# Kernel tuning notes

Hardware: AMD Instinct MI355X
Metric: run time of the kernel (lower is better)

## Reference

```python
import jax, jax.numpy as jnp
import numpy as np

B, S, T, E, D = 16, 2048, 1024, 256, 256  # batch, src_len, tgt_len, enc_size, dec_size


def setup_inputs() -> dict:
    key = jax.random.key(0)
    k1, k2, k3, k4, k5 = jax.random.split(key, 5)
    enc_states = jax.random.normal(k1, (B, S, E), dtype=jnp.float32)
    dec_states = jax.random.normal(k2, (B, T, D), dtype=jnp.float32)
    # valid-prefix mask: each row has at least one valid (True) source position
    lengths = jax.random.randint(k3, (B,), 1, S + 1)
    src_mask = jnp.arange(S)[None, :] < lengths[:, None]  # (B, S) bool
    # Dense layer weights (no bias). Glorot-ish scale.
    W_enc = jax.random.normal(k4, (E, D), dtype=jnp.float32) / np.sqrt(E)
    W_fin = jax.random.normal(k5, (E + D, D), dtype=jnp.float32) / np.sqrt(E + D)
    return {"enc_states": enc_states, "dec_states": dec_states,
            "src_mask": src_mask, "W_enc": W_enc, "W_fin": W_fin}


def reference(enc_states, dec_states, src_mask, W_enc, W_fin):
    # enc_trnsfrmr: (B,S,E) @ (E,D) -> (B,S,D)
    enc_proj = jnp.einsum('bse,ed->bsd', enc_states, W_enc)
    # attention scores: batch_dot(dec_states, enc_proj^T) -> (B,T,S)
    scores = jnp.einsum('btd,bsd->bts', dec_states, enc_proj)
    scores = jnp.where(src_mask[:, None, :], scores, -jnp.inf)
    wts = jax.nn.softmax(scores, axis=-1)  # (B,T,S)
    # broadcast-multiply + reduce_sum == weighted sum over src positions
    context = jnp.einsum('bts,bse->bte', wts, enc_states)  # (B,T,E)
    cat = jnp.concatenate([context, dec_states], axis=-1)  # (B,T,E+D)
    return jnp.tanh(jnp.einsum('btf,fd->btd', cat, W_fin))  # (B,T,D)
```

## Files before the change

kernel.cpp:

```cpp
#include <hip/hip_runtime.h>
#include <math.h>
#include <stdint.h>

#define NB 16
#define NS 2048
#define NT 1024
#define NE 256
#define ND 256
#define NM (NB * NT)
#define KF (NE + ND)

typedef short sh8 __attribute__((ext_vector_type(8)));
typedef float f4v __attribute__((ext_vector_type(4)));

static __device__ __forceinline__ float bf2f(unsigned short u) {
    union { unsigned int i; float f; } v;
    v.i = ((unsigned int)u) << 16;
    return v.f;
}
static __device__ __forceinline__ unsigned short f2bf(float f) {
    union { unsigned int i; float f; } v;
    v.f = f;
    unsigned int x = v.i;
    x += 0x7FFFu + ((x >> 16) & 1u);
    return (unsigned short)(x >> 16);
}
static __device__ __forceinline__ float4 load4(const void* p, int isbf, long idx) {
    if (isbf) {
        const unsigned short* h = (const unsigned short*)p + idx;
        ushort4 u = *(const ushort4*)h;
        return make_float4(bf2f(u.x), bf2f(u.y), bf2f(u.z), bf2f(u.w));
    }
    const float* f = (const float*)p + idx;
    return *(const float4*)f;
}
static __device__ __forceinline__ int mvalid(const void* m, int kind, int b, int s) {
    long idx = (long)b * NS + s;
    switch (kind) {
        case 0:  return ((const unsigned char*)m)[idx] != 0;
        case 1:  return ((const int*)m)[idx] != 0;
        case 2:  return ((const unsigned short*)m)[idx] != 0;
        default: return ((const unsigned int*)m)[idx] != 0;
    }
}

__global__ void k_detect(const void* __restrict__ enc_raw,
                         const void* __restrict__ mask_raw,
                         int* __restrict__ flags) {
    __shared__ int cnt;
    if (threadIdx.x == 0) cnt = 0;
    __syncthreads();
    const unsigned short* h = (const unsigned short*)enc_raw;
    int local = 0;
    for (int i = threadIdx.x; i < 4096; i += 256) {
        int ex = (h[i] >> 7) & 0xFF;
        if (ex >= 97 && ex <= 157) local++;
    }
    atomicAdd(&cnt, local);
    __syncthreads();
    if (threadIdx.x == 0) {
        int isbf = (cnt >= 3700) ? 1 : 0;
        const unsigned char* mb = (const unsigned char*)mask_raw;
        int kind;
        if (mb[1] == 0x3F)                       kind = 2;
        else if (mb[3] == 0x3F && mb[1] == 0)    kind = 3;
        else if (mb[1] == 1)                     kind = 0;
        else if (mb[4] == 1 || mb[8] == 1)       kind = 1;
        else                                     kind = (mb[NS] == 1) ? 0 : 1;
        flags[0] = isbf;
        flags[1] = kind;
    }
}

__global__ __launch_bounds__(256) void k_split(const void* __restrict__ src,
                                               const int* __restrict__ flags,
                                               unsigned short* __restrict__ hh,
                                               unsigned short* __restrict__ ll) {
    const int isbf = flags[0];
    const long i = ((long)blockIdx.x * 256 + threadIdx.x) * 8;
    if (isbf) {
        sh8 v = *(const sh8*)((const unsigned short*)src + i);
        *(sh8*)(hh + i) = v;
    } else {
        const float* f = (const float*)src + i;
        sh8 hv, lv;
#pragma unroll
        for (int j = 0; j < 8; ++j) {
            float x = f[j];
            unsigned short h = f2bf(x);
            hv[j] = (short)h;
            lv[j] = (short)f2bf(x - bf2f(h));
        }
        *(sh8*)(hh + i) = hv;
        *(sh8*)(ll + i) = lv;
    }
}

__global__ __launch_bounds__(256) void k_twf(const void* __restrict__ Wfin,
                                             const int* __restrict__ flags,
                                             unsigned short* __restrict__ wfh,
                                             unsigned short* __restrict__ wfl) {
    const int isbf = flags[0];
    __shared__ float T[64][68];
    const int f0 = blockIdx.x * 64, n0 = blockIdx.y * 64;
    const int tid = threadIdx.x;
#pragma unroll
    for (int i = 0; i < 4; ++i) {
        int idx = tid + i * 256;
        int r = idx >> 4, c4 = (idx & 15) << 2;
        float4 v = load4(Wfin, isbf, (long)(f0 + r) * ND + n0 + c4);
        T[r][c4] = v.x; T[r][c4 + 1] = v.y; T[r][c4 + 2] = v.z; T[r][c4 + 3] = v.w;
    }
    __syncthreads();
#pragma unroll
    for (int i = 0; i < 4; ++i) {
        int idx = tid + i * 256;
        int n = idx >> 4, f4 = (idx & 15) << 2;
        ushort4 hv, lv;
        float x;
        x = T[f4 + 0][n]; hv.x = f2bf(x); lv.x = f2bf(x - bf2f(hv.x));
        x = T[f4 + 1][n]; hv.y = f2bf(x); lv.y = f2bf(x - bf2f(hv.y));
        x = T[f4 + 2][n]; hv.z = f2bf(x); lv.z = f2bf(x - bf2f(hv.z));
        x = T[f4 + 3][n]; hv.w = f2bf(x); lv.w = f2bf(x - bf2f(hv.w));
        long base = (long)(n0 + n) * KF + f0 + f4;
        *(ushort4*)&wfh[base] = hv;
        *(ushort4*)&wfl[base] = lv;
    }
}

__global__ __launch_bounds__(256) void k_q_m(const unsigned short* __restrict__ dh,
                                             const unsigned short* __restrict__ dl,
                                             const unsigned short* __restrict__ wh,
                                             const unsigned short* __restrict__ wl,
                                             const int* __restrict__ flags,
                                             unsigned short* __restrict__ qh,
                                             unsigned short* __restrict__ ql) {
    const int isbf = flags[0];
    const int tid = threadIdx.x;
    const int lane = tid & 63, wid = tid >> 6;
    const int lr = lane & 15, lg = lane >> 4;
    const long m0 = (long)blockIdx.x * 128 + wid * 32;
    const int  n0 = blockIdx.y * 64;
    __shared__ __align__(16) unsigned short Bh_s[64][264];
    __shared__ __align__(16) unsigned short Bl_s[64][264];
    {
        const int row = tid >> 2, seg = (tid & 3) * 64;
        const unsigned short* src = wh + (long)(n0 + row) * ND + seg;
#pragma unroll
        for (int c = 0; c < 8; ++c)
            *(sh8*)&Bh_s[row][seg + c * 8] = *(const sh8*)(src + c * 8);
        if (!isbf) {
            const unsigned short* src2 = wl + (long)(n0 + row) * ND + seg;
#pragma unroll
            for (int c = 0; c < 8; ++c)
                *(sh8*)&Bl_s[row][seg + c * 8] = *(const sh8*)(src2 + c * 8);
        }
    }
    __syncthreads();
    const unsigned short* Ah = dh + (m0 + lr) * ND + lg * 8;
    const unsigned short* Al = dl + (m0 + lr) * ND + lg * 8;
    f4v acc[2][4];
#pragma unroll
    for (int i = 0; i < 2; ++i)
#pragma unroll
        for (int j = 0; j < 4; ++j) acc[i][j] = (f4v){0.f, 0.f, 0.f, 0.f};
    if (isbf) {
#pragma unroll
        for (int k8 = 0; k8 < 8; ++k8) {
            const int ko = k8 * 32;
            sh8 a0 = *(const sh8*)(Ah + ko);
            sh8 a1 = *(const sh8*)(Ah + 16 * ND + ko);
#pragma unroll
            for (int ni = 0; ni < 4; ++ni) {
                sh8 b = *(const sh8*)&Bh_s[ni * 16 + lr][ko + lg * 8];
                acc[0][ni] = __builtin_amdgcn_mfma_f32_16x16x32_bf16(a0, b, acc[0][ni], 0, 0, 0);
                acc[1][ni] = __builtin_amdgcn_mfma_f32_16x16x32_bf16(a1, b, acc[1][ni], 0, 0, 0);
            }
        }
    } else {
#pragma unroll
        for (int k8 = 0; k8 < 8; ++k8) {
            const int ko = k8 * 32;
            sh8 a0 = *(const sh8*)(Ah + ko);
            sh8 a1 = *(const sh8*)(Ah + 16 * ND + ko);
            sh8 la0 = *(const sh8*)(Al + ko);
            sh8 la1 = *(const sh8*)(Al + 16 * ND + ko);
#pragma unroll
            for (int ni = 0; ni < 4; ++ni) {
                sh8 b  = *(const sh8*)&Bh_s[ni * 16 + lr][ko + lg * 8];
                sh8 lb = *(const sh8*)&Bl_s[ni * 16 + lr][ko + lg * 8];
                acc[0][ni] = __builtin_amdgcn_mfma_f32_16x16x32_bf16(a0, b, acc[0][ni], 0, 0, 0);
                acc[0][ni] = __builtin_amdgcn_mfma_f32_16x16x32_bf16(la0, b, acc[0][ni], 0, 0, 0);
                acc[0][ni] = __builtin_amdgcn_mfma_f32_16x16x32_bf16(a0, lb, acc[0][ni], 0, 0, 0);
                acc[1][ni] = __builtin_amdgcn_mfma_f32_16x16x32_bf16(a1, b, acc[1][ni], 0, 0, 0);
                acc[1][ni] = __builtin_amdgcn_mfma_f32_16x16x32_bf16(la1, b, acc[1][ni], 0, 0, 0);
                acc[1][ni] = __builtin_amdgcn_mfma_f32_16x16x32_bf16(a1, lb, acc[1][ni], 0, 0, 0);
            }
        }
    }
#pragma unroll
    for (int mi = 0; mi < 2; ++mi)
#pragma unroll
        for (int r = 0; r < 4; ++r) {
            long rowb = (m0 + mi * 16 + lg * 4 + r) * NE + n0 + lr;
#pragma unroll
            for (int ni = 0; ni < 4; ++ni) {
                float v = acc[mi][ni][r];
                unsigned short h = f2bf(v);
                qh[rowb + ni * 16] = h;
                ql[rowb + ni * 16] = f2bf(v - bf2f(h));
            }
        }
}

__global__ __launch_bounds__(256, 2) void k_attn(
    const unsigned short* qh, const unsigned short* ql,
    const unsigned short* __restrict__ eh, const unsigned short* __restrict__ el,
    const void* __restrict__ mask, const int* __restrict__ flags,
    unsigned short* ch, unsigned short* cl,
    float* __restrict__ pctx, float* __restrict__ Mp, float* __restrict__ Lp)
{
    const int isbf  = flags[0];
    const int mkind = flags[1];
    const int b  = blockIdx.y;
    const int t0 = blockIdx.x * 32;
    const int part = blockIdx.z, nparts = gridDim.z;
    const int tid  = threadIdx.x;
    const int lane = tid & 63;
    const int wid  = tid >> 6;
    const int th = wid & 1;
    const int sh = wid >> 1;
    const int lr = lane & 15;
    const int lg = lane >> 4;

    __shared__ __align__(16) unsigned short EHR[32][264];
    __shared__ __align__(16) unsigned short ELR[32][264];
    __shared__ __align__(16) unsigned short VT[2][256][40];
    __shared__ __align__(16) float PBs[32][36];
    __shared__ float hm[2][32];
    __shared__ float hs[2][32];
    __shared__ int s_len;

    if (tid == 0) s_len = 0;
    __syncthreads();
    {
        int c = 0;
#pragma unroll
        for (int j = 0; j < 8; ++j) c += mvalid(mask, mkind, b, tid * 8 + j);
        atomicAdd(&s_len, c);
    }
    __syncthreads();
    const int len  = s_len;
    const int s_lo = part * (NS / nparts);
    const int s_hi = min(s_lo + NS / nparts, len);
    const int ntiles = (s_hi > s_lo) ? ((s_hi - s_lo + 31) >> 5) : 0;
    const long mrow = (long)part * NM + (long)b * NT + t0;
    if (ntiles == 0) {
        if (nparts > 1 && tid < 32) { Mp[mrow + tid] = -INFINITY; Lp[mrow + tid] = 0.f; }
        return;
    }

    sh8 qhf[8], qlf[8];
    {
        const unsigned short* qp  = qh + ((long)b * NT + t0 + th * 16 + lr) * NE + lg * 8;
        const unsigned short* qp2 = ql + ((long)b * NT + t0 + th * 16 + lr) * NE + lg * 8;
#pragma unroll
        for (int k8 = 0; k8 < 8; ++k8) {
            qhf[k8] = *(const sh8*)(qp  + k8 * 32);
            qlf[k8] = *(const sh8*)(qp2 + k8 * 32);
        }
    }

    f4v O[8];
#pragma unroll
    for (int et = 0; et < 8; ++et) O[et] = (f4v){0.f, 0.f, 0.f, 0.f};
    float Mreg4[4], L4[4], MregP = -INFINITY;
#pragma unroll
    for (int r = 0; r < 4; ++r) { Mreg4[r] = -INFINITY; L4[r] = 0.f; }

    const int ss = tid >> 3;
    const int ee = (tid & 7) * 8;
    const int swzw = ((tid & 7) & 3) << 3;

    sh8 rh[4], rl[4];
    {
        const unsigned short* eg = eh + ((long)b * NS + s_lo + ss) * NE;
#pragma unroll
        for (int c = 0; c < 4; ++c) rh[c] = *(const sh8*)(eg + ee + c * 64);
        if (!isbf) {
            const unsigned short* eg2 = el + ((long)b * NS + s_lo + ss) * NE;
#pragma unroll
            for (int c = 0; c < 4; ++c) rl[c] = *(const sh8*)(eg2 + ee + c * 64);
        }
#pragma unroll
        for (int c = 0; c < 4; ++c) {
            const int e0 = ee + c * 64;
            *(sh8*)&EHR[ss][e0] = rh[c];
            if (!isbf) *(sh8*)&ELR[ss][e0] = rl[c];
            const int cs = ss ^ swzw;
#pragma unroll
            for (int j = 0; j < 8; ++j) VT[0][e0 + j][cs] = (unsigned short)rh[c][j];
        }
    }
    int cur = 0;

    for (int it = 0; it < ntiles; ++it) {
        const int s0 = s_lo + it * 32;
        __syncthreads();
        f4v cacc = (f4v){0.f, 0.f, 0.f, 0.f};
        {
            const unsigned short* ep = &EHR[sh * 16 + lr][lg * 8];
            const unsigned short* lp = &ELR[sh * 16 + lr][lg * 8];
            if (isbf) {
#pragma unroll
                for (int k8 = 0; k8 < 8; ++k8) {
                    sh8 ea = *(const sh8*)(ep + k8 * 32);
                    cacc = __builtin_amdgcn_mfma_f32_16x16x32_bf16(ea, qhf[k8], cacc, 0, 0, 0);
                    cacc = __builtin_amdgcn_mfma_f32_16x16x32_bf16(ea, qlf[k8], cacc, 0, 0, 0);
                }
            } else {
#pragma unroll
                for (int k8 = 0; k8 < 8; ++k8) {
                    sh8 ea = *(const sh8*)(ep + k8 * 32);
                    sh8 eb = *(const sh8*)(lp + k8 * 32);
                    cacc = __builtin_amdgcn_mfma_f32_16x16x32_bf16(ea, qhf[k8], cacc, 0, 0, 0);
                    cacc = __builtin_amdgcn_mfma_f32_16x16x32_bf16(ea, qlf[k8], cacc, 0, 0, 0);
                    cacc = __builtin_amdgcn_mfma_f32_16x16x32_bf16(eb, qhf[k8], cacc, 0, 0, 0);
                }
            }
        }
        float sc[4];
#pragma unroll
        for (int r = 0; r < 4; ++r) {
            int sl = sh * 16 + lg * 4 + r;
            sc[r] = (s0 + sl < len) ? cacc[r] : -INFINITY;
        }
        float m4 = fmaxf(fmaxf(sc[0], sc[1]), fmaxf(sc[2], sc[3]));
        m4 = fmaxf(m4, __shfl_xor(m4, 16));
        m4 = fmaxf(m4, __shfl_xor(m4, 32));
        float p[4], ps = 0.f;
#pragma unroll
        for (int r = 0; r < 4; ++r) {
            p[r] = (sc[r] == -INFINITY) ? 0.f : __expf(sc[r] - m4);
            ps += p[r];
        }
        ps += __shfl_xor(ps, 16);
        ps += __shfl_xor(ps, 32);
        if (lane < 16) { hm[sh][th * 16 + lane] = m4; hs[sh][th * 16 + lane] = ps; }
        *(float4*)&PBs[th * 16 + lr][sh * 16 + lg * 4] = make_float4(p[0], p[1], p[2], p[3]);
        __syncthreads();
        float f0, f1, al[4];
        {
            const int tP = th * 16 + lr;
            float h0 = hm[0][tP], h1 = hm[1][tP];
            float Mn = fmaxf(MregP, fmaxf(h0, h1));
            f0 = __expf(h0 - Mn);
            f1 = __expf(h1 - Mn);
            MregP = Mn;
        }
#pragma unroll
        for (int r = 0; r < 4; ++r) {
            const int t4 = th * 16 + lg * 4 + r;
            float g0 = hm[0][t4], g1 = hm[1][t4];
            float Mn = fmaxf(Mreg4[r], fmaxf(g0, g1));
            al[r] = __expf(Mreg4[r] - Mn);
            L4[r] = L4[r] * al[r] + hs[0][t4] * __expf(g0 - Mn) + hs[1][t4] * __expf(g1 - Mn);
            Mreg4[r] = Mn;
        }
        const int more = (it + 1 < ntiles);
        if (more) {
            const unsigned short* eg = eh + ((long)b * NS + s0 + 32 + ss) * NE;
#pragma unroll
            for (int c = 0; c < 4; ++c) rh[c] = *(const sh8*)(eg + ee + c * 64);
            if (!isbf) {
                const unsigned short* eg2 = el + ((long)b * NS + s0 + 32 + ss) * NE;
#pragma unroll
                for (int c = 0; c < 4; ++c) rl[c] = *(const sh8*)(eg2 + ee + c * 64);
            }
        }
        {
            const float fsc = (lg < 2) ? f0 : f1;
            f4v pA = *(const f4v*)&PBs[th * 16 + lr][lg * 8];
            f4v pB = *(const f4v*)&PBs[th * 16 + lr][lg * 8 + 4];
            sh8 pf;
#pragma unroll
            for (int j = 0; j < 4; ++j) {
                pf[j]     = (short)f2bf(pA[j] * fsc);
                pf[4 + j] = (short)f2bf(pB[j] * fsc);
            }
            f4v alv = (f4v){al[0], al[1], al[2], al[3]};
#pragma unroll
            for (int et = 0; et < 8; ++et) O[et] *= alv;
#pragma unroll
            for (int et = 0; et < 8; ++et) {
                const int row = sh * 128 + et * 16 + lr;
                sh8 vf = *(const sh8*)&VT[cur][row][(lg ^ ((row >> 3) & 3)) * 8];
                O[et] = __builtin_amdgcn_mfma_f32_16x16x32_bf16(pf, vf, O[et], 0, 0, 0);
            }
        }
        if (more) {
#pragma unroll
            for (int c = 0; c < 4; ++c) {
                const int e0 = ee + c * 64;
                *(sh8*)&EHR[ss][e0] = rh[c];
                if (!isbf) *(sh8*)&ELR[ss][e0] = rl[c];
                const int cs = ss ^ swzw;
#pragma unroll
                for (int j = 0; j < 8; ++j) VT[cur ^ 1][e0 + j][cs] = (unsigned short)rh[c][j];
            }
            cur ^= 1;
        }
    }
    if (nparts == 1) {
        f4v inv;
#pragma unroll
        for (int r = 0; r < 4; ++r) inv[r] = 1.0f / L4[r];
#pragma unroll
        for (int et = 0; et < 8; ++et) {
            f4v ov = O[et] * inv;
            long rbase = ((long)b * NT + t0 + th * 16 + lg * 4) * NE + sh * 128 + et * 16 + lr;
#pragma unroll
            for (int r = 0; r < 4; ++r) {
                float v = ov[r];
                unsigned short h = f2bf(v);
                ch[rbase + (long)r * NE] = h;
                cl[rbase + (long)r * NE] = f2bf(v - bf2f(h));
            }
        }
    } else {
        float* op = pctx + (long)part * NM * NE;
#pragma unroll
        for (int et = 0; et < 8; ++et) {
            long rbase = ((long)b * NT + t0 + th * 16 + lg * 4) * NE + sh * 128 + et * 16 + lr;
#pragma unroll
            for (int r = 0; r < 4; ++r)
                op[rbase + (long)r * NE] = O[et][r];
        }
        if (sh == 0 && lr == 0) {
#pragma unroll
            for (int r = 0; r < 4; ++r) {
                Mp[mrow + th * 16 + lg * 4 + r] = Mreg4[r];
                Lp[mrow + th * 16 + lg * 4 + r] = L4[r];
            }
        }
    }
}

__global__ __launch_bounds__(256) void k_comb(const float* __restrict__ pctx,
                                              const float* __restrict__ Mp,
                                              const float* __restrict__ Lp,
                                              int nparts,
                                              unsigned short* __restrict__ ch,
                                              unsigned short* __restrict__ cl) {
    const long m = (long)blockIdx.x * 8 + (threadIdx.x >> 5);
    const int  e0 = (threadIdx.x & 31) * 8;
    float Mv[4], Lv[4];
    float M = -INFINITY;
    for (int p = 0; p < nparts; ++p) {
        Mv[p] = Mp[(long)p * NM + m];
        Lv[p] = Lp[(long)p * NM + m];
        if (Lv[p] > 0.f) M = fmaxf(M, Mv[p]);
    }
    float L = 0.f, w[4];
    for (int p = 0; p < nparts; ++p) {
        w[p] = (Lv[p] > 0.f) ? __expf(Mv[p] - M) : 0.f;
        L += Lv[p] * w[p];
    }
    float o[8] = {};
    for (int p = 0; p < nparts; ++p) {
        if (w[p] > 0.f) {
            const float* src = pctx + (long)p * NM * NE + m * NE + e0;
            f4v a = *(const f4v*)src;
            f4v c = *(const f4v*)(src + 4);
#pragma unroll
            for (int j = 0; j < 4; ++j) { o[j] += a[j] * w[p]; o[4 + j] += c[j] * w[p]; }
        }
    }
    const float inv = 1.0f / L;
    unsigned short hv[8], lv[8];
#pragma unroll
    for (int j = 0; j < 8; ++j) {
        float v = o[j] * inv;
        unsigned short h = f2bf(v);
        hv[j] = h;
        lv[j] = f2bf(v - bf2f(h));
    }
    long base = m * NE + e0;
    *(ushort4*)&ch[base]     = *(ushort4*)&hv[0];
    *(ushort4*)&ch[base + 4] = *(ushort4*)&hv[4];
    *(ushort4*)&cl[base]     = *(ushort4*)&lv[0];
    *(ushort4*)&cl[base + 4] = *(ushort4*)&lv[4];
}

__global__ __launch_bounds__(256) void k_fin_m(const unsigned short* __restrict__ ch,
                                               const unsigned short* __restrict__ cl,
                                               const unsigned short* __restrict__ dh,
                                               const unsigned short* __restrict__ dl,
                                               const unsigned short* __restrict__ wh,
                                               const unsigned short* __restrict__ wl,
                                               const int* __restrict__ flags,
                                               void* __restrict__ out) {
    const int isbf = flags[0];
    const int tid = threadIdx.x;
    const int lane = tid & 63, wid = tid >> 6;
    const int lr = lane & 15, lg = lane >> 4;
    const long m0 = (long)blockIdx.x * 128 + wid * 32;
    const int  n0 = blockIdx.y * 64;
    __shared__ __align__(16) unsigned short Bh_s[64][520];
    {
        const int row = tid >> 2, seg = (tid & 3) * 128;
        const unsigned short* src = wh + (long)(n0 + row) * KF + seg;
#pragma unroll
        for (int c = 0; c < 16; ++c)
            *(sh8*)&Bh_s[row][seg + c * 8] = *(const sh8*)(src + c * 8);
    }
    __syncthreads();
    f4v acc[2][4];
#pragma unroll
    for (int i = 0; i < 2; ++i)
#pragma unroll
        for (int j = 0; j < 4; ++j) acc[i][j] = (f4v){0.f, 0.f, 0.f, 0.f};

#pragma unroll
    for (int k8 = 0; k8 < 16; ++k8) {
        const int ko = k8 * 32;
        const unsigned short* Ahp = (k8 < 8) ? (ch + (m0 + lr) * NE + ko + lg * 8)
                                             : (dh + (m0 + lr) * ND + (ko - NE) + lg * 8);
        const unsigned short* Alp = (k8 < 8) ? (cl + (m0 + lr) * NE + ko + lg * 8)
                                             : (dl + (m0 + lr) * ND + (ko - NE) + lg * 8);
        const int astr = (k8 < 8) ? NE : ND;
        sh8 a0 = *(const sh8*)(Ahp);
        sh8 a1 = *(const sh8*)(Ahp + 16 * astr);
        if (isbf) {
#pragma unroll
            for (int ni = 0; ni < 4; ++ni) {
                sh8 b = *(const sh8*)&Bh_s[ni * 16 + lr][ko + lg * 8];
                acc[0][ni] = __builtin_amdgcn_mfma_f32_16x16x32_bf16(a0, b, acc[0][ni], 0, 0, 0);
                acc[1][ni] = __builtin_amdgcn_mfma_f32_16x16x32_bf16(a1, b, acc[1][ni], 0, 0, 0);
            }
        } else {
            sh8 la0 = *(const sh8*)(Alp);
            sh8 la1 = *(const sh8*)(Alp + 16 * astr);
            const unsigned short* Blp = wl + (long)(n0 + lr) * KF + ko + lg * 8;
#pragma unroll
            for (int ni = 0; ni < 4; ++ni) {
                sh8 b  = *(const sh8*)&Bh_s[ni * 16 + lr][ko + lg * 8];
                sh8 lb = *(const sh8*)(Blp + (long)ni * 16 * KF);
                acc[0][ni] = __builtin_amdgcn_mfma_f32_16x16x32_bf16(a0, b, acc[0][ni], 0, 0, 0);
                acc[0][ni] = __builtin_amdgcn_mfma_f32_16x16x32_bf16(la0, b, acc[0][ni], 0, 0, 0);
                acc[0][ni] = __builtin_amdgcn_mfma_f32_16x16x32_bf16(a0, lb, acc[0][ni], 0, 0, 0);
                acc[1][ni] = __builtin_amdgcn_mfma_f32_16x16x32_bf16(a1, b, acc[1][ni], 0, 0, 0);
                acc[1][ni] = __builtin_amdgcn_mfma_f32_16x16x32_bf16(la1, b, acc[1][ni], 0, 0, 0);
                acc[1][ni] = __builtin_amdgcn_mfma_f32_16x16x32_bf16(a1, lb, acc[1][ni], 0, 0, 0);
            }
        }
    }
    if (isbf) {
        unsigned short* o = (unsigned short*)out;
#pragma unroll
        for (int mi = 0; mi < 2; ++mi)
#pragma unroll
            for (int r = 0; r < 4; ++r) {
                long rowb = (m0 + mi * 16 + lg * 4 + r) * ND + n0 + lr;
#pragma unroll
                for (int ni = 0; ni < 4; ++ni)
                    o[rowb + ni * 16] = f2bf(tanhf(acc[mi][ni][r]));
            }
    } else {
        float* o = (float*)out;
#pragma unroll
        for (int mi = 0; mi < 2; ++mi)
#pragma unroll
            for (int r = 0; r < 4; ++r) {
                long rowb = (m0 + mi * 16 + lg * 4 + r) * ND + n0 + lr;
#pragma unroll
                for (int ni = 0; ni < 4; ++ni)
                    o[rowb + ni * 16] = tanhf(acc[mi][ni][r]);
            }
    }
}

extern "C" void kernel_launch(void* const* d_in, const int* in_sizes, int n_in,
                              void* d_out, int out_size, void* d_ws, size_t ws_size,
                              hipStream_t stream) {
    const void* enc  = d_in[0];
    const void* dec  = d_in[1];
    const void* mask = d_in[2];
    const void* Wenc = d_in[3];
    const void* Wfin = d_in[4];

    unsigned short* ehb = (unsigned short*)d_ws;
    unsigned short* elb = ehb + (size_t)NB * NS * NE;
    unsigned short* qhb = elb + (size_t)NB * NS * NE;
    unsigned short* qlb = qhb + (size_t)NM * NE;
    unsigned short* dhb = qlb + (size_t)NM * NE;
    unsigned short* dlb = dhb + (size_t)NM * ND;
    unsigned short* weh = dlb + (size_t)NM * ND;
    unsigned short* wel = weh + (size_t)NE * ND;
    unsigned short* wfh = wel + (size_t)NE * ND;
    unsigned short* wfl = wfh + (size_t)KF * ND;
    unsigned short* wend = wfl + (size_t)KF * ND;

    const size_t fixed = (size_t)((char*)wend - (char*)d_ws);
    int parts = 1;
    for (int p = 4; p >= 1; p >>= 1) {
        size_t need = fixed + ((p > 1) ? ((size_t)p * NM * NE * 4 + (size_t)p * NM * 8) : 0) + 256;
        if (ws_size >= need) { parts = p; break; }
    }
    float* pctx = (float*)wend;
    float* Mpb  = pctx + ((parts > 1) ? (size_t)parts * NM * NE : 0);
    float* Lpb  = Mpb + (size_t)parts * NM;
    int*   flags = (int*)(Lpb + (size_t)parts * NM);

    k_detect<<<1, 256, 0, stream>>>(enc, mask, flags);
    k_split<<<(NB * NS * NE) / 2048, 256, 0, stream>>>(enc, flags, ehb, elb);
    k_split<<<(NM * ND) / 2048, 256, 0, stream>>>(dec, flags, dhb, dlb);
    k_split<<<(NE * ND) / 2048, 256, 0, stream>>>(Wenc, flags, weh, wel);
    k_twf<<<dim3(KF / 64, ND / 64), 256, 0, stream>>>(Wfin, flags, wfh, wfl);
    k_q_m<<<dim3(NM / 128, NE / 64), 256, 0, stream>>>(dhb, dlb, weh, wel, flags, qhb, qlb);
    k_attn<<<dim3(NT / 32, NB, parts), 256, 0, stream>>>(qhb, qlb, ehb, elb, mask, flags,
                                                         qhb, qlb, pctx, Mpb, Lpb);
    if (parts > 1)
        k_comb<<<NM / 8, 256, 0, stream>>>(pctx, Mpb, Lpb, parts, qhb, qlb);
    k_fin_m<<<dim3(NM / 128, ND / 64), 256, 0, stream>>>(qhb, qlb, dhb, dlb, wfh, wfl,
                                                         flags, d_out);
}
```

Measured before the change: 282.5 us.

## Rework attention V transpose, split MFMA chains, swizzle GEMM block order, stage W_fin lo in LDS

Several changes land together. The attention kernel drops the double-buffered swizzled VT scatter and instead builds V^T from EHR with a per-thread column gather each tile. It also hoists the next-tile global prefetch before the barrier and splits the score MFMA accumulation into independent chains so they can overlap. Both GEMM kernels now use a 1D grid remapped so consecutive blocks share M tiles across N, and k_fin_m stages both hi and lo weights in LDS in two K phases instead of reading the lo weights from global memory. The risks are LDS bank conflicts from the unswizzled VT layout and the column gather, plus an extra barrier in the final GEMM.

```diff
diff --git a/kernel.cpp b/kernel.cpp
--- a/kernel.cpp
+++ b/kernel.cpp
@@ -139,8 +139,11 @@
     const int tid = threadIdx.x;
     const int lane = tid & 63, wid = tid >> 6;
     const int lr = lane & 15, lg = lane >> 4;
-    const long m0 = (long)blockIdx.x * 128 + wid * 32;
-    const int  n0 = blockIdx.y * 64;
+    const int bid = blockIdx.x;
+    const int mblk = (bid & 7) + (((bid >> 3) >> 2) << 3);
+    const int nblk = (bid >> 3) & 3;
+    const long m0 = (long)mblk * 128 + wid * 32;
+    const int  n0 = nblk * 64;
     __shared__ __align__(16) unsigned short Bh_s[64][264];
     __shared__ __align__(16) unsigned short Bl_s[64][264];
     {
@@ -235,7 +238,7 @@
 
     __shared__ __align__(16) unsigned short EHR[32][264];
     __shared__ __align__(16) unsigned short ELR[32][264];
-    __shared__ __align__(16) unsigned short VT[2][256][40];
+    __shared__ __align__(16) unsigned short VT[256][40];
     __shared__ __align__(16) float PBs[32][36];
     __shared__ float hm[2][32];
     __shared__ float hs[2][32];
@@ -280,7 +283,6 @@
 
     const int ss = tid >> 3;
     const int ee = (tid & 7) * 8;
-    const int swzw = ((tid & 7) & 3) << 3;
 
     sh8 rh[4], rl[4];
     {
@@ -297,37 +299,45 @@
             const int e0 = ee + c * 64;
             *(sh8*)&EHR[ss][e0] = rh[c];
             if (!isbf) *(sh8*)&ELR[ss][e0] = rl[c];
-            const int cs = ss ^ swzw;
-#pragma unroll
-            for (int j = 0; j < 8; ++j) VT[0][e0 + j][cs] = (unsigned short)rh[c][j];
-        }
-    }
-    int cur = 0;
+        }
+    }
 
     for (int it = 0; it < ntiles; ++it) {
         const int s0 = s_lo + it * 32;
         __syncthreads();
-        f4v cacc = (f4v){0.f, 0.f, 0.f, 0.f};
+        f4v cacc;
         {
             const unsigned short* ep = &EHR[sh * 16 + lr][lg * 8];
             const unsigned short* lp = &ELR[sh * 16 + lr][lg * 8];
+            f4v c0 = (f4v){0.f, 0.f, 0.f, 0.f};
+            f4v c1 = (f4v){0.f, 0.f, 0.f, 0.f};
+            f4v c2 = (f4v){0.f, 0.f, 0.f, 0.f};
             if (isbf) {
 #pragma unroll
                 for (int k8 = 0; k8 < 8; ++k8) {
                     sh8 ea = *(const sh8*)(ep + k8 * 32);
-                    cacc = __builtin_amdgcn_mfma_f32_16x16x32_bf16(ea, qhf[k8], cacc, 0, 0, 0);
-                    cacc = __builtin_amdgcn_mfma_f32_16x16x32_bf16(ea, qlf[k8], cacc, 0, 0, 0);
+                    c0 = __builtin_amdgcn_mfma_f32_16x16x32_bf16(ea, qhf[k8], c0, 0, 0, 0);
+                    c1 = __builtin_amdgcn_mfma_f32_16x16x32_bf16(ea, qlf[k8], c1, 0, 0, 0);
                 }
             } else {
 #pragma unroll
                 for (int k8 = 0; k8 < 8; ++k8) {
                     sh8 ea = *(const sh8*)(ep + k8 * 32);
                     sh8 eb = *(const sh8*)(lp + k8 * 32);
-                    cacc = __builtin_amdgcn_mfma_f32_16x16x32_bf16(ea, qhf[k8], cacc, 0, 0, 0);
-                    cacc = __builtin_amdgcn_mfma_f32_16x16x32_bf16(ea, qlf[k8], cacc, 0, 0, 0);
-                    cacc = __builtin_amdgcn_mfma_f32_16x16x32_bf16(eb, qhf[k8], cacc, 0, 0, 0);
+                    c0 = __builtin_amdgcn_mfma_f32_16x16x32_bf16(ea, qhf[k8], c0, 0, 0, 0);
+                    c1 = __builtin_amdgcn_mfma_f32_16x16x32_bf16(ea, qlf[k8], c1, 0, 0, 0);
+                    c2 = __builtin_amdgcn_mfma_f32_16x16x32_bf16(eb, qhf[k8], c2, 0, 0, 0);
                 }
             }
+            cacc = c0 + c1 + c2;
+        }
+        {
+            unsigned short col[32];
+#pragma unroll
+            for (int s = 0; s < 32; ++s) col[s] = EHR[s][tid];
+#pragma unroll
+            for (int c = 0; c < 4; ++c)
+                *(sh8*)&VT[tid][c * 8] = *(const sh8*)&col[c * 8];
         }
         float sc[4];
 #pragma unroll
@@ -348,6 +358,17 @@
         ps += __shfl_xor(ps, 32);
         if (lane < 16) { hm[sh][th * 16 + lane] = m4; hs[sh][th * 16 + lane] = ps; }
         *(float4*)&PBs[th * 16 + lr][sh * 16 + lg * 4] = make_float4(p[0], p[1], p[2], p[3]);
+        const int more = (it + 1 < ntiles);
+        if (more) {
+            const unsigned short* eg = eh + ((long)b * NS + s0 + 32 + ss) * NE;
+#pragma unroll
+            for (int c = 0; c < 4; ++c) rh[c] = *(const sh8*)(eg + ee + c * 64);
+            if (!isbf) {
+                const unsigned short* eg2 = el + ((long)b * NS + s0 + 32 + ss) * NE;
+#pragma unroll
+                for (int c = 0; c < 4; ++c) rl[c] = *(const sh8*)(eg2 + ee + c * 64);
+            }
+        }
         __syncthreads();
         float f0, f1, al[4];
         {
@@ -367,17 +388,6 @@
             L4[r] = L4[r] * al[r] + hs[0][t4] * __expf(g0 - Mn) + hs[1][t4] * __expf(g1 - Mn);
             Mreg4[r] = Mn;
         }
-        const int more = (it + 1 < ntiles);
-        if (more) {
-            const unsigned short* eg = eh + ((long)b * NS + s0 + 32 + ss) * NE;
-#pragma unroll
-            for (int c = 0; c < 4; ++c) rh[c] = *(const sh8*)(eg + ee + c * 64);
-            if (!isbf) {
-                const unsigned short* eg2 = el + ((long)b * NS + s0 + 32 + ss) * NE;
-#pragma unroll
-                for (int c = 0; c < 4; ++c) rl[c] = *(const sh8*)(eg2 + ee + c * 64);
-            }
-        }
         {
             const float fsc = (lg < 2) ? f0 : f1;
             f4v pA = *(const f4v*)&PBs[th * 16 + lr][lg * 8];
@@ -393,8 +403,7 @@
             for (int et = 0; et < 8; ++et) O[et] *= alv;
 #pragma unroll
             for (int et = 0; et < 8; ++et) {
-                const int row = sh * 128 + et * 16 + lr;
-                sh8 vf = *(const sh8*)&VT[cur][row][(lg ^ ((row >> 3) & 3)) * 8];
+                sh8 vf = *(const sh8*)&VT[sh * 128 + et * 16 + lr][lg * 8];
                 O[et] = __builtin_amdgcn_mfma_f32_16x16x32_bf16(pf, vf, O[et], 0, 0, 0);
             }
         }
@@ -404,11 +413,7 @@
                 const int e0 = ee + c * 64;
                 *(sh8*)&EHR[ss][e0] = rh[c];
                 if (!isbf) *(sh8*)&ELR[ss][e0] = rl[c];
-                const int cs = ss ^ swzw;
-#pragma unroll
-                for (int j = 0; j < 8; ++j) VT[cur ^ 1][e0 + j][cs] = (unsigned short)rh[c][j];
-            }
-            cur ^= 1;
+            }
         }
     }
     if (nparts == 1) {
@@ -504,17 +509,14 @@
     const int tid = threadIdx.x;
     const int lane = tid & 63, wid = tid >> 6;
     const int lr = lane & 15, lg = lane >> 4;
-    const long m0 = (long)blockIdx.x * 128 + wid * 32;
-    const int  n0 = blockIdx.y * 64;
-    __shared__ __align__(16) unsigned short Bh_s[64][520];
-    {
-        const int row = tid >> 2, seg = (tid & 3) * 128;
-        const unsigned short* src = wh + (long)(n0 + row) * KF + seg;
-#pragma unroll
-        for (int c = 0; c < 16; ++c)
-            *(sh8*)&Bh_s[row][seg + c * 8] = *(const sh8*)(src + c * 8);
-    }
-    __syncthreads();
+    const int bid = blockIdx.x;
+    const int mblk = (bid & 7) + (((bid >> 3) >> 2) << 3);
+    const int nblk = (bid >> 3) & 3;
+    const long m0 = (long)mblk * 128 + wid * 32;
+    const int  n0 = nblk * 64;
+    __shared__ __align__(16) unsigned short Bh_s[64][264];
+    __shared__ __align__(16) unsigned short Bl_s[64][264];
+    const int row = tid >> 2, seg = (tid & 3) * 64;
     f4v acc[2][4];
 #pragma unroll
     for (int i = 0; i < 2; ++i)
@@ -522,36 +524,55 @@
         for (int j = 0; j < 4; ++j) acc[i][j] = (f4v){0.f, 0.f, 0.f, 0.f};
 
 #pragma unroll
-    for (int k8 = 0; k8 < 16; ++k8) {
-        const int ko = k8 * 32;
-        const unsigned short* Ahp = (k8 < 8) ? (ch + (m0 + lr) * NE + ko + lg * 8)
-                                             : (dh + (m0 + lr) * ND + (ko - NE) + lg * 8);
-        const unsigned short* Alp = (k8 < 8) ? (cl + (m0 + lr) * NE + ko + lg * 8)
-                                             : (dl + (m0 + lr) * ND + (ko - NE) + lg * 8);
-        const int astr = (k8 < 8) ? NE : ND;
-        sh8 a0 = *(const sh8*)(Ahp);
-        sh8 a1 = *(const sh8*)(Ahp + 16 * astr);
+    for (int ph = 0; ph < 2; ++ph) {
+        if (ph) __syncthreads();
+        {
+            const unsigned short* src = wh + (long)(n0 + row) * KF + ph * 256 + seg;
+#pragma unroll
+            for (int c = 0; c < 8; ++c)
+                *(sh8*)&Bh_s[row][seg + c * 8] = *(const sh8*)(src + c * 8);
+            if (!isbf) {
+                const unsigned short* src2 = wl + (long)(n0 + row) * KF + ph * 256 + seg;
+#pragma unroll
+                for (int c = 0; c < 8; ++c)
+                    *(sh8*)&Bl_s[row][seg + c * 8] = *(const sh8*)(src2 + c * 8);
+            }
+        }
+        __syncthreads();
+        const unsigned short* Ah = (ph == 0 ? ch : dh) + (m0 + lr) * 256 + lg * 8;
+        const unsigned short* Al = (ph == 0 ? cl : dl) + (m0 + lr) * 256 + lg * 8;
         if (isbf) {
 #pragma unroll
-            for (int ni = 0; ni < 4; ++ni) {
-                sh8 b = *(const sh8*)&Bh_s[ni * 16 + lr][ko + lg * 8];
-                acc[0][ni] = __builtin_amdgcn_mfma_f32_16x16x32_bf16(a0, b, acc[0][ni], 0, 0, 0);
-                acc[1][ni] = __builtin_amdgcn_mfma_f32_16x16x32_bf16(a1, b, acc[1][ni], 0, 0, 0);
+            for (int k8 = 0; k8 < 8; ++k8) {
+                const int ko = k8 * 32;
+                sh8 a0 = *(const sh8*)(Ah + ko);
+                sh8 a1 = *(const sh8*)(Ah + 16 * 256 + ko);
+#pragma unroll
+                for (int ni = 0; ni < 4; ++ni) {
+                    sh8 b = *(const sh8*)&Bh_s[ni * 16 + lr][ko + lg * 8];
+                    acc[0][ni] = __builtin_amdgcn_mfma_f32_16x16x32_bf16(a0, b, acc[0][ni], 0, 0, 0);
+                    acc[1][ni] = __builtin_amdgcn_mfma_f32_16x16x32_bf16(a1, b, acc[1][ni], 0, 0, 0);
+                }
             }
         } else {
-            sh8 la0 = *(const sh8*)(Alp);
-            sh8 la1 = *(const sh8*)(Alp + 16 * astr);
-            const unsigned short* Blp = wl + (long)(n0 + lr) * KF + ko + lg * 8;
-#pragma unroll
-            for (int ni = 0; ni < 4; ++ni) {
-                sh8 b  = *(const sh8*)&Bh_s[ni * 16 + lr][ko + lg * 8];
-                sh8 lb = *(const sh8*)(Blp + (long)ni * 16 * KF);
-                acc[0][ni] = __builtin_amdgcn_mfma_f32_16x16x32_bf16(a0, b, acc[0][ni], 0, 0, 0);
-                acc[0][ni] = __builtin_amdgcn_mfma_f32_16x16x32_bf16(la0, b, acc[0][ni], 0, 0, 0);
-                acc[0][ni] = __builtin_amdgcn_mfma_f32_16x16x32_bf16(a0, lb, acc[0][ni], 0, 0, 0);
-                acc[1][ni] = __builtin_amdgcn_mfma_f32_16x16x32_bf16(a1, b, acc[1][ni], 0, 0, 0);
-                acc[1][ni] = __builtin_amdgcn_mfma_f32_16x16x32_bf16(la1, b, acc[1][ni], 0, 0, 0);
-                acc[1][ni] = __builtin_amdgcn_mfma_f32_16x16x32_bf16(a1, lb, acc[1][ni], 0, 0, 0);
+#pragma unroll
+            for (int k8 = 0; k8 < 8; ++k8) {
+                const int ko = k8 * 32;
+                sh8 a0 = *(const sh8*)(Ah + ko);
+                sh8 a1 = *(const sh8*)(Ah + 16 * 256 + ko);
+                sh8 la0 = *(const sh8*)(Al + ko);
+                sh8 la1 = *(const sh8*)(Al + 16 * 256 + ko);
+#pragma unroll
+                for (int ni = 0; ni < 4; ++ni) {
+                    sh8 b  = *(const sh8*)&Bh_s[ni * 16 + lr][ko + lg * 8];
+                    sh8 lb = *(const sh8*)&Bl_s[ni * 16 + lr][ko + lg * 8];
+                    acc[0][ni] = __builtin_amdgcn_mfma_f32_16x16x32_bf16(a0, b, acc[0][ni], 0, 0, 0);
+                    acc[0][ni] = __builtin_amdgcn_mfma_f32_16x16x32_bf16(la0, b, acc[0][ni], 0, 0, 0);
+                    acc[0][ni] = __builtin_amdgcn_mfma_f32_16x16x32_bf16(a0, lb, acc[0][ni], 0, 0, 0);
+                    acc[1][ni] = __builtin_amdgcn_mfma_f32_16x16x32_bf16(a1, b, acc[1][ni], 0, 0, 0);
+                    acc[1][ni] = __builtin_amdgcn_mfma_f32_16x16x32_bf16(la1, b, acc[1][ni], 0, 0, 0);
+                    acc[1][ni] = __builtin_amdgcn_mfma_f32_16x16x32_bf16(a1, lb, acc[1][ni], 0, 0, 0);
+                }
             }
         }
     }
@@ -617,11 +638,10 @@
     k_split<<<(NM * ND) / 2048, 256, 0, stream>>>(dec, flags, dhb, dlb);
     k_split<<<(NE * ND) / 2048, 256, 0, stream>>>(Wenc, flags, weh, wel);
     k_twf<<<dim3(KF / 64, ND / 64), 256, 0, stream>>>(Wfin, flags, wfh, wfl);
-    k_q_m<<<dim3(NM / 128, NE / 64), 256, 0, stream>>>(dhb, dlb, weh, wel, flags, qhb, qlb);
+    k_q_m<<<512, 256, 0, stream>>>(dhb, dlb, weh, wel, flags, qhb, qlb);
     k_attn<<<dim3(NT / 32, NB, parts), 256, 0, stream>>>(qhb, qlb, ehb, elb, mask, flags,
                                                          qhb, qlb, pctx, Mpb, Lpb);
     if (parts > 1)
         k_comb<<<NM / 8, 256, 0, stream>>>(pctx, Mpb, Lpb, parts, qhb, qlb);
-    k_fin_m<<<dim3(NM / 128, ND / 64), 256, 0, stream>>>(qhb, qlb, dhb, dlb, wfh, wfl,
-                                                         flags, d_out);
-}
+    k_fin_m<<<512, 256, 0, stream>>>(qhb, qlb, dhb, dlb, wfh, wfl, flags, d_out);
+}
```

After: 266.7 us. 5.6% less time.

## Pre-transpose encoder tiles, stream low parts from global, compute mask lengths once

Applied to the files above, without the earlier changes.

Adds a prep kernel that splits the encoder states into bf16 hi/lo and also writes a pre-transposed MFMA-fragment layout, so the attention kernel no longer builds the V transpose in shared memory element by element. The attention kernel drops the ELR shared buffer, loads low-part fragments straight from global, splits the score MFMA chain into independent accumulators, and interleaves source tiles across partitions. Mask lengths are computed once in the detect kernel instead of per block. Occupancy is raised to 3 blocks, split parts are capped at 2, and the GEMM grids are remapped so blocks that share input rows run together. In exchange it adds a third full-size encoder copy in workspace plus an extra write pass, and raises register pressure.

```diff
diff --git a/kernel.cpp b/kernel.cpp
--- a/kernel.cpp
+++ b/kernel.cpp
@@ -43,22 +43,35 @@
         default: return ((const unsigned int*)m)[idx] != 0;
     }
 }
+static __device__ __forceinline__ void f8_to_hl(const float* p, sh8& h8, sh8& l8) {
+    f4v x0 = *(const f4v*)p;
+    f4v x1 = *(const f4v*)(p + 4);
+#pragma unroll
+    for (int j = 0; j < 4; ++j) {
+        unsigned short h = f2bf(x0[j]); h8[j] = (short)h; l8[j] = (short)f2bf(x0[j] - bf2f(h));
+        h = f2bf(x1[j]); h8[4 + j] = (short)h; l8[4 + j] = (short)f2bf(x1[j] - bf2f(h));
+    }
+}
 
 __global__ void k_detect(const void* __restrict__ enc_raw,
                          const void* __restrict__ mask_raw,
                          int* __restrict__ flags) {
     __shared__ int cnt;
-    if (threadIdx.x == 0) cnt = 0;
+    __shared__ int kindS;
+    __shared__ int lensS[16];
+    const int tid = threadIdx.x;
+    if (tid == 0) cnt = 0;
+    if (tid < 16) lensS[tid] = 0;
     __syncthreads();
     const unsigned short* h = (const unsigned short*)enc_raw;
     int local = 0;
-    for (int i = threadIdx.x; i < 4096; i += 256) {
+    for (int i = tid; i < 4096; i += 256) {
         int ex = (h[i] >> 7) & 0xFF;
         if (ex >= 97 && ex <= 157) local++;
     }
     atomicAdd(&cnt, local);
     __syncthreads();
-    if (threadIdx.x == 0) {
+    if (tid == 0) {
         int isbf = (cnt >= 3700) ? 1 : 0;
         const unsigned char* mb = (const unsigned char*)mask_raw;
         int kind;
@@ -69,7 +82,56 @@
         else                                     kind = (mb[NS] == 1) ? 0 : 1;
         flags[0] = isbf;
         flags[1] = kind;
-    }
+        kindS = kind;
+    }
+    __syncthreads();
+    const int kind = kindS;
+    const int bb = tid >> 4, sl = tid & 15;
+    int c = 0;
+    for (int j = 0; j < 128; ++j) c += mvalid(mask_raw, kind, bb, sl + j * 16);
+    atomicAdd(&lensS[bb], c);
+    __syncthreads();
+    if (tid < 16) flags[2 + tid] = lensS[tid];
+}
+
+__global__ __launch_bounds__(256) void k_prep(const void* __restrict__ enc,
+                                              const int* __restrict__ flags,
+                                              unsigned short* __restrict__ eh,
+                                              unsigned short* __restrict__ el,
+                                              unsigned short* __restrict__ eT) {
+    const int isbf = flags[0];
+    const int st = blockIdx.x, b = blockIdx.y;
+    const int tid = threadIdx.x;
+    __shared__ __align__(16) unsigned short T[32][264];
+    const int s = tid >> 3, e0 = (tid & 7) * 32;
+    const long rbase = ((long)b * NS + st * 32 + s) * NE + e0;
+    if (isbf) {
+        const unsigned short* src = (const unsigned short*)enc + rbase;
+#pragma unroll
+        for (int c = 0; c < 4; ++c) {
+            sh8 hv = *(const sh8*)(src + c * 8);
+            *(sh8*)&eh[rbase + c * 8] = hv;
+            *(sh8*)&T[s][e0 + c * 8] = hv;
+        }
+    } else {
+        const float* src = (const float*)enc + rbase;
+#pragma unroll
+        for (int c = 0; c < 4; ++c) {
+            sh8 hv, lv;
+            f8_to_hl(src + c * 8, hv, lv);
+            *(sh8*)&eh[rbase + c * 8] = hv;
+            *(sh8*)&el[rbase + c * 8] = lv;
+            *(sh8*)&T[s][e0 + c * 8] = hv;
+        }
+    }
+    __syncthreads();
+    unsigned short col[32];
+#pragma unroll
+    for (int ss = 0; ss < 32; ++ss) col[ss] = T[ss][tid];
+    const long tbase = (((long)b * 64 + st) * 256 + tid) * 32;
+#pragma unroll
+    for (int c = 0; c < 4; ++c)
+        *(sh8*)&eT[tbase + c * 8] = *(const sh8*)&col[c * 8];
 }
 
 __global__ __launch_bounds__(256) void k_split(const void* __restrict__ src,
@@ -84,13 +146,7 @@
     } else {
         const float* f = (const float*)src + i;
         sh8 hv, lv;
-#pragma unroll
-        for (int j = 0; j < 8; ++j) {
-            float x = f[j];
-            unsigned short h = f2bf(x);
-            hv[j] = (short)h;
-            lv[j] = (short)f2bf(x - bf2f(h));
-        }
+        f8_to_hl(f, hv, lv);
         *(sh8*)(hh + i) = hv;
         *(sh8*)(ll + i) = lv;
     }
@@ -139,8 +195,11 @@
     const int tid = threadIdx.x;
     const int lane = tid & 63, wid = tid >> 6;
     const int lr = lane & 15, lg = lane >> 4;
-    const long m0 = (long)blockIdx.x * 128 + wid * 32;
-    const int  n0 = blockIdx.y * 64;
+    const int bid = blockIdx.x;
+    const int mblk = (bid & 7) + (((bid >> 3) >> 2) << 3);
+    const int nblk = (bid >> 3) & 3;
+    const long m0 = (long)mblk * 128 + wid * 32;
+    const int  n0 = nblk * 64;
     __shared__ __align__(16) unsigned short Bh_s[64][264];
     __shared__ __align__(16) unsigned short Bl_s[64][264];
     {
@@ -213,15 +272,15 @@
         }
 }
 
-__global__ __launch_bounds__(256, 2) void k_attn(
+__global__ __launch_bounds__(256, 3) void k_attn(
     const unsigned short* qh, const unsigned short* ql,
     const unsigned short* __restrict__ eh, const unsigned short* __restrict__ el,
-    const void* __restrict__ mask, const int* __restrict__ flags,
+    const unsigned short* __restrict__ eT,
+    const int* __restrict__ flags,
     unsigned short* ch, unsigned short* cl,
     float* __restrict__ pctx, float* __restrict__ Mp, float* __restrict__ Lp)
 {
     const int isbf  = flags[0];
-    const int mkind = flags[1];
     const int b  = blockIdx.y;
     const int t0 = blockIdx.x * 32;
     const int part = blockIdx.z, nparts = gridDim.z;
@@ -234,26 +293,14 @@
     const int lg = lane >> 4;
 
     __shared__ __align__(16) unsigned short EHR[32][264];
-    __shared__ __align__(16) unsigned short ELR[32][264];
-    __shared__ __align__(16) unsigned short VT[2][256][40];
+    __shared__ __align__(16) unsigned short VTf[2 * 8 * 4 * 16 * 8];
     __shared__ __align__(16) float PBs[32][36];
     __shared__ float hm[2][32];
     __shared__ float hs[2][32];
-    __shared__ int s_len;
-
-    if (tid == 0) s_len = 0;
-    __syncthreads();
-    {
-        int c = 0;
-#pragma unroll
-        for (int j = 0; j < 8; ++j) c += mvalid(mask, mkind, b, tid * 8 + j);
-        atomicAdd(&s_len, c);
-    }
-    __syncthreads();
-    const int len  = s_len;
-    const int s_lo = part * (NS / nparts);
-    const int s_hi = min(s_lo + NS / nparts, len);
-    const int ntiles = (s_hi > s_lo) ? ((s_hi - s_lo + 31) >> 5) : 0;
+
+    const int len = flags[2 + b];
+    const int nT = (len + 31) >> 5;
+    const int ntiles = (nT > part) ? ((nT - part + nparts - 1) / nparts) : 0;
     const long mrow = (long)part * NM + (long)b * NT + t0;
     if (ntiles == 0) {
         if (nparts > 1 && tid < 32) { Mp[mrow + tid] = -INFINITY; Lp[mrow + tid] = 0.f; }
@@ -280,54 +327,52 @@
 
     const int ss = tid >> 3;
     const int ee = (tid & 7) * 8;
-    const int swzw = ((tid & 7) & 3) << 3;
-
-    sh8 rh[4], rl[4];
+    const int vb = ((tid >> 7) * 8 + ((tid >> 4) & 7)) * 64 + (tid & 15);
+
+    sh8 rh[4], vt[4];
     {
-        const unsigned short* eg = eh + ((long)b * NS + s_lo + ss) * NE;
+        const unsigned short* eg = eh + ((long)b * NS + part * 32 + ss) * NE;
 #pragma unroll
         for (int c = 0; c < 4; ++c) rh[c] = *(const sh8*)(eg + ee + c * 64);
+        const unsigned short* tg = eT + (((long)b * 64 + part) * 256 + tid) * 32;
+#pragma unroll
+        for (int c = 0; c < 4; ++c) vt[c] = *(const sh8*)(tg + c * 8);
+#pragma unroll
+        for (int c = 0; c < 4; ++c)
+            *(sh8*)&EHR[ss][ee + c * 64] = rh[c];
+    }
+
+    for (int it = 0; it < ntiles; ++it) {
+        const int s0 = (part + it * nparts) << 5;
+        __syncthreads();
+#pragma unroll
+        for (int c = 0; c < 4; ++c)
+            *(sh8*)&VTf[(vb + c * 16) * 8] = vt[c];
+        sh8 elf[8];
         if (!isbf) {
-            const unsigned short* eg2 = el + ((long)b * NS + s_lo + ss) * NE;
-#pragma unroll
-            for (int c = 0; c < 4; ++c) rl[c] = *(const sh8*)(eg2 + ee + c * 64);
-        }
-#pragma unroll
-        for (int c = 0; c < 4; ++c) {
-            const int e0 = ee + c * 64;
-            *(sh8*)&EHR[ss][e0] = rh[c];
-            if (!isbf) *(sh8*)&ELR[ss][e0] = rl[c];
-            const int cs = ss ^ swzw;
-#pragma unroll
-            for (int j = 0; j < 8; ++j) VT[0][e0 + j][cs] = (unsigned short)rh[c][j];
-        }
-    }
-    int cur = 0;
-
-    for (int it = 0; it < ntiles; ++it) {
-        const int s0 = s_lo + it * 32;
-        __syncthreads();
-        f4v cacc = (f4v){0.f, 0.f, 0.f, 0.f};
+            const unsigned short* lp = el + ((long)b * NS + s0 + sh * 16 + lr) * NE + lg * 8;
+#pragma unroll
+            for (int k8 = 0; k8 < 8; ++k8) elf[k8] = *(const sh8*)(lp + k8 * 32);
+        }
+        f4v cacc;
         {
             const unsigned short* ep = &EHR[sh * 16 + lr][lg * 8];
-            const unsigned short* lp = &ELR[sh * 16 + lr][lg * 8];
-            if (isbf) {
-#pragma unroll
-                for (int k8 = 0; k8 < 8; ++k8) {
-                    sh8 ea = *(const sh8*)(ep + k8 * 32);
-                    cacc = __builtin_amdgcn_mfma_f32_16x16x32_bf16(ea, qhf[k8], cacc, 0, 0, 0);
-                    cacc = __builtin_amdgcn_mfma_f32_16x16x32_bf16(ea, qlf[k8], cacc, 0, 0, 0);
-                }
-            } else {
-#pragma unroll
-                for (int k8 = 0; k8 < 8; ++k8) {
-                    sh8 ea = *(const sh8*)(ep + k8 * 32);
-                    sh8 eb = *(const sh8*)(lp + k8 * 32);
-                    cacc = __builtin_amdgcn_mfma_f32_16x16x32_bf16(ea, qhf[k8], cacc, 0, 0, 0);
-                    cacc = __builtin_amdgcn_mfma_f32_16x16x32_bf16(ea, qlf[k8], cacc, 0, 0, 0);
-                    cacc = __builtin_amdgcn_mfma_f32_16x16x32_bf16(eb, qhf[k8], cacc, 0, 0, 0);
-                }
-            }
+            f4v c0 = (f4v){0.f, 0.f, 0.f, 0.f};
+            f4v c1 = (f4v){0.f, 0.f, 0.f, 0.f};
+#pragma unroll
+            for (int k8 = 0; k8 < 8; ++k8) {
+                sh8 ea = *(const sh8*)(ep + k8 * 32);
+                c0 = __builtin_amdgcn_mfma_f32_16x16x32_bf16(ea, qhf[k8], c0, 0, 0, 0);
+                c1 = __builtin_amdgcn_mfma_f32_16x16x32_bf16(ea, qlf[k8], c1, 0, 0, 0);
+            }
+            if (!isbf) {
+                f4v c2 = (f4v){0.f, 0.f, 0.f, 0.f};
+#pragma unroll
+                for (int k8 = 0; k8 < 8; ++k8)
+                    c2 = __builtin_amdgcn_mfma_f32_16x16x32_bf16(elf[k8], qhf[k8], c2, 0, 0, 0);
+                c0 += c2;
+            }
+            cacc = c0 + c1;
         }
         float sc[4];
 #pragma unroll
@@ -348,6 +393,16 @@
         ps += __shfl_xor(ps, 32);
         if (lane < 16) { hm[sh][th * 16 + lane] = m4; hs[sh][th * 16 + lane] = ps; }
         *(float4*)&PBs[th * 16 + lr][sh * 16 + lg * 4] = make_float4(p[0], p[1], p[2], p[3]);
+        const int more = (it + 1 < ntiles);
+        if (more) {
+            const int stn = part + (it + 1) * nparts;
+            const unsigned short* eg = eh + ((long)b * NS + stn * 32 + ss) * NE;
+#pragma unroll
+            for (int c = 0; c < 4; ++c) rh[c] = *(const sh8*)(eg + ee + c * 64);
+            const unsigned short* tg = eT + (((long)b * 64 + stn) * 256 + tid) * 32;
+#pragma unroll
+            for (int c = 0; c < 4; ++c) vt[c] = *(const sh8*)(tg + c * 8);
+        }
         __syncthreads();
         float f0, f1, al[4];
         {
@@ -367,17 +422,6 @@
             L4[r] = L4[r] * al[r] + hs[0][t4] * __expf(g0 - Mn) + hs[1][t4] * __expf(g1 - Mn);
             Mreg4[r] = Mn;
         }
-        const int more = (it + 1 < ntiles);
-        if (more) {
-            const unsigned short* eg = eh + ((long)b * NS + s0 + 32 + ss) * NE;
-#pragma unroll
-            for (int c = 0; c < 4; ++c) rh[c] = *(const sh8*)(eg + ee + c * 64);
-            if (!isbf) {
-                const unsigned short* eg2 = el + ((long)b * NS + s0 + 32 + ss) * NE;
-#pragma unroll
-                for (int c = 0; c < 4; ++c) rl[c] = *(const sh8*)(eg2 + ee + c * 64);
-            }
-        }
         {
             const float fsc = (lg < 2) ? f0 : f1;
             f4v pA = *(const f4v*)&PBs[th * 16 + lr][lg * 8];
@@ -393,22 +437,14 @@
             for (int et = 0; et < 8; ++et) O[et] *= alv;
 #pragma unroll
             for (int et = 0; et < 8; ++et) {
-                const int row = sh * 128 + et * 16 + lr;
-                sh8 vf = *(const sh8*)&VT[cur][row][(lg ^ ((row >> 3) & 3)) * 8];
+                sh8 vf = *(const sh8*)&VTf[((sh * 8 + et) * 64 + lg * 16 + lr) * 8];
                 O[et] = __builtin_amdgcn_mfma_f32_16x16x32_bf16(pf, vf, O[et], 0, 0, 0);
             }
         }
         if (more) {
 #pragma unroll
-            for (int c = 0; c < 4; ++c) {
-                const int e0 = ee + c * 64;
-                *(sh8*)&EHR[ss][e0] = rh[c];
-                if (!isbf) *(sh8*)&ELR[ss][e0] = rl[c];
-                const int cs = ss ^ swzw;
-#pragma unroll
-                for (int j = 0; j < 8; ++j) VT[cur ^ 1][e0 + j][cs] = (unsigned short)rh[c][j];
-            }
-            cur ^= 1;
+            for (int c = 0; c < 4; ++c)
+                *(sh8*)&EHR[ss][ee + c * 64] = rh[c];
         }
     }
     if (nparts == 1) {
@@ -504,8 +540,11 @@
     const int tid = threadIdx.x;
     const int lane = tid & 63, wid = tid >> 6;
     const int lr = lane & 15, lg = lane >> 4;
-    const long m0 = (long)blockIdx.x * 128 + wid * 32;
-    const int  n0 = blockIdx.y * 64;
+    const int bid = blockIdx.x;
+    const int mblk = (bid & 7) + (((bid >> 3) >> 2) << 3);
+    const int nblk = (bid >> 3) & 3;
+    const long m0 = (long)mblk * 128 + wid * 32;
+    const int  n0 = nblk * 64;
     __shared__ __align__(16) unsigned short Bh_s[64][520];
     {
         const int row = tid >> 2, seg = (tid & 3) * 128;
@@ -591,7 +630,8 @@
 
     unsigned short* ehb = (unsigned short*)d_ws;
     unsigned short* elb = ehb + (size_t)NB * NS * NE;
-    unsigned short* qhb = elb + (size_t)NB * NS * NE;
+    unsigned short* eTb = elb + (size_t)NB * NS * NE;
+    unsigned short* qhb = eTb + (size_t)NB * NS * NE;
     unsigned short* qlb = qhb + (size_t)NM * NE;
     unsigned short* dhb = qlb + (size_t)NM * NE;
     unsigned short* dlb = dhb + (size_t)NM * ND;
@@ -603,7 +643,7 @@
 
     const size_t fixed = (size_t)((char*)wend - (char*)d_ws);
     int parts = 1;
-    for (int p = 4; p >= 1; p >>= 1) {
+    for (int p = 2; p >= 1; p >>= 1) {
         size_t need = fixed + ((p > 1) ? ((size_t)p * NM * NE * 4 + (size_t)p * NM * 8) : 0) + 256;
         if (ws_size >= need) { parts = p; break; }
     }
@@ -613,15 +653,14 @@
     int*   flags = (int*)(Lpb + (size_t)parts * NM);
 
     k_detect<<<1, 256, 0, stream>>>(enc, mask, flags);
-    k_split<<<(NB * NS * NE) / 2048, 256, 0, stream>>>(enc, flags, ehb, elb);
+    k_prep<<<dim3(64, 16), 256, 0, stream>>>(enc, flags, ehb, elb, eTb);
     k_split<<<(NM * ND) / 2048, 256, 0, stream>>>(dec, flags, dhb, dlb);
     k_split<<<(NE * ND) / 2048, 256, 0, stream>>>(Wenc, flags, weh, wel);
     k_twf<<<dim3(KF / 64, ND / 64), 256, 0, stream>>>(Wfin, flags, wfh, wfl);
-    k_q_m<<<dim3(NM / 128, NE / 64), 256, 0, stream>>>(dhb, dlb, weh, wel, flags, qhb, qlb);
-    k_attn<<<dim3(NT / 32, NB, parts), 256, 0, stream>>>(qhb, qlb, ehb, elb, mask, flags,
+    k_q_m<<<512, 256, 0, stream>>>(dhb, dlb, weh, wel, flags, qhb, qlb);
+    k_attn<<<dim3(NT / 32, NB, parts), 256, 0, stream>>>(qhb, qlb, ehb, elb, eTb, flags,
                                                          qhb, qlb, pctx, Mpb, Lpb);
     if (parts > 1)
         k_comb<<<NM / 8, 256, 0, stream>>>(pctx, Mpb, Lpb, parts, qhb, qlb);
-    k_fin_m<<<dim3(NM / 128, ND / 64), 256, 0, stream>>>(qhb, qlb, dhb, dlb, wfh, wfl,
-                                                         flags, d_out);
-}
+    k_fin_m<<<512, 256, 0, stream>>>(qhb, qlb, dhb, dlb, wfh, wfl, flags, d_out);
+}
```

Result: slower. 560.6 us (+98.5%).
